# Optimization experiments

Measured on AMD Instinct MI355X. Metric: run time of the kernel, lower is better.

Reference implementation:

```python
import jax, jax.numpy as jnp
import numpy as np
from jax import lax

J = 2  # number of decomposition levels (init arg)


def afb1d(x, h0, h1, axis):
    """1D analysis filter bank along `axis` (2=D, 3=H, 4=W) of NCDHW x.
    h0/h1 are length-L time-reversed filters (cross-correlation weights),
    matching the reversed buffers stored by prep_filt_afb3d.
    Returns (N, 2C, ...) with channel layout (C, [lo, hi]).
    """
    C = x.shape[1]
    L = h0.shape[0]
    n = x.shape[axis]
    # pywt.dwt_coeff_len(n, L, mode='zero') == floor((n + L - 1) / 2)
    outsize = (n + L - 1) // 2
    p = 2 * (outsize - 1) - n + L
    pads = [(0, 0)] * 3
    # torch code: if p odd, pad 1 extra at the END of the axis, then p//2 both sides
    pads[axis - 2] = (p // 2, p // 2 + (p % 2))
    # depthwise weight: interleaved [lo_c, hi_c] per channel group -> (2C, 1, kD, kH, kW)
    w = jnp.tile(jnp.stack([h0, h1]), (C, 1))  # (2C, L)
    kshape = [1, 1, 1]
    kshape[axis - 2] = L
    w = w.reshape(2 * C, 1, *kshape)
    strides = [1, 1, 1]
    strides[axis - 2] = 2
    return lax.conv_general_dilated(
        x, w,
        window_strides=tuple(strides),
        padding=pads,
        feature_group_count=C,
        dimension_numbers=('NCDHW', 'OIDHW', 'NCDHW'),
    )


def dwt3d_level(x, h0, h1):
    """Single-level 3D DWT: row (W), then col (H), then depth (D) filtering."""
    y = afb1d(x, h0, h1, 4)   # along W -> channels (C, 2w)
    y = afb1d(y, h0, h1, 3)   # along H -> channels (C, 2w, 2h)
    y = afb1d(y, h0, h1, 2)   # along D -> channels (C, 2w, 2h, 2d)
    s = y.shape
    y = y.reshape(s[0], -1, 8, s[2], s[3], s[4])  # (N, C, 8, D', H', W')
    low = y[:, :, 0]        # LLL
    highs = y[:, :, 1:]     # 7 high subbands
    return low, highs


def setup_inputs() -> dict:
    key = jax.random.key(0)
    x = jax.random.normal(key, (2, 4, 128, 128, 128), dtype=jnp.float32)
    s = np.float32(1.0 / np.sqrt(2.0))
    # db1 analysis filters, time-reversed (as stored by prep_filt_afb3d):
    # pywt dec_lo=[s,s] -> reversed [s,s]; dec_hi=[-s,s] -> reversed [s,-s]
    h0 = jnp.asarray(np.array([s, s], dtype=np.float32))
    h1 = jnp.asarray(np.array([s, -s], dtype=np.float32))
    return {"x": x, "h0": h0, "h1": h1}


def reference(x, h0, h1):
    ll = x
    yh = []
    for _ in range(J):
        ll, high = dwt3d_level(ll, h0, h1)
        yh.append(high)
    # (lowpass, highs_level0, highs_level1)
    return (ll, *yh)
```

## Files before the change

kernel.cpp:

```cpp
#include <hip/hip_runtime.h>

#define DIM 128
#define NCV 8

__global__ __launch_bounds__(256)
void haar3d_fused(const float* __restrict__ x,
                  const float* __restrict__ h0,
                  const float* __restrict__ h1,
                  float* __restrict__ ll2,
                  float* __restrict__ hi1,
                  float* __restrict__ hi2)
{
    __shared__ float2 lds[4 * 4 * 16];

    const int tw = blockIdx.x;
    const int th = blockIdx.y;
    const int td = blockIdx.z & 15;
    const int nc = blockIdx.z >> 4;

    const int tid = threadIdx.x;
    const int sw2 = tid & 15;
    const int sh  = (tid >> 4) & 3;
    const int sd  = tid >> 6;

    const float g00 = h0[0], g01 = h0[1];
    const float g10 = h1[0], g11 = h1[1];

    const int gd = td * 8 + 2 * sd;
    const int gh = th * 8 + 2 * sh;
    const int gw = tw * 64 + 4 * sw2;

    const float* base = x + ((((long)nc * DIM + gd) * DIM + gh) * DIM + gw);

    float4 q[2][2];
    q[0][0] = *reinterpret_cast<const float4*>(base);
    q[0][1] = *reinterpret_cast<const float4*>(base + DIM);
    q[1][0] = *reinterpret_cast<const float4*>(base + DIM * DIM);
    q[1][1] = *reinterpret_cast<const float4*>(base + DIM * DIM + DIM);

    float Lw[2][2][2], Hw[2][2][2];
#pragma unroll
    for (int i = 0; i < 2; ++i)
#pragma unroll
        for (int j = 0; j < 2; ++j) {
            const float4 v = q[i][j];
            Lw[i][j][0] = g00 * v.x + g01 * v.y;
            Hw[i][j][0] = g10 * v.x + g11 * v.y;
            Lw[i][j][1] = g00 * v.z + g01 * v.w;
            Hw[i][j][1] = g10 * v.z + g11 * v.w;
        }

    float LL[2][2], LH[2][2], HL[2][2], HH[2][2];
#pragma unroll
    for (int i = 0; i < 2; ++i)
#pragma unroll
        for (int s = 0; s < 2; ++s) {
            LL[i][s] = g00 * Lw[i][0][s] + g01 * Lw[i][1][s];
            LH[i][s] = g10 * Lw[i][0][s] + g11 * Lw[i][1][s];
            HL[i][s] = g00 * Hw[i][0][s] + g01 * Hw[i][1][s];
            HH[i][s] = g10 * Hw[i][0][s] + g11 * Hw[i][1][s];
        }

    float LLL[2], LLH[2], LHL[2], LHH[2], HLL[2], HLH[2], HHL[2], HHH[2];
#pragma unroll
    for (int s = 0; s < 2; ++s) {
        LLL[s] = g00 * LL[0][s] + g01 * LL[1][s];
        LLH[s] = g10 * LL[0][s] + g11 * LL[1][s];
        LHL[s] = g00 * LH[0][s] + g01 * LH[1][s];
        LHH[s] = g10 * LH[0][s] + g11 * LH[1][s];
        HLL[s] = g00 * HL[0][s] + g01 * HL[1][s];
        HLH[s] = g10 * HL[0][s] + g11 * HL[1][s];
        HHL[s] = g00 * HH[0][s] + g01 * HH[1][s];
        HHH[s] = g10 * HH[0][s] + g11 * HH[1][s];
    }

    const int d1  = td * 4 + sd;
    const int h1c = th * 4 + sh;
    const int w1  = tw * 32 + 2 * sw2;

    {
        const long S1 = 64L * 64 * 64;
        const long sp = ((long)d1 * 64 + h1c) * 64 + w1;
        float* hb = hi1 + (long)nc * 7 * S1 + sp;
        *reinterpret_cast<float2*>(hb + 0 * S1) = make_float2(LLH[0], LLH[1]);
        *reinterpret_cast<float2*>(hb + 1 * S1) = make_float2(LHL[0], LHL[1]);
        *reinterpret_cast<float2*>(hb + 2 * S1) = make_float2(LHH[0], LHH[1]);
        *reinterpret_cast<float2*>(hb + 3 * S1) = make_float2(HLL[0], HLL[1]);
        *reinterpret_cast<float2*>(hb + 4 * S1) = make_float2(HLH[0], HLH[1]);
        *reinterpret_cast<float2*>(hb + 5 * S1) = make_float2(HHL[0], HHL[1]);
        *reinterpret_cast<float2*>(hb + 6 * S1) = make_float2(HHH[0], HHH[1]);
    }

    lds[(sd * 4 + sh) * 16 + sw2] = make_float2(LLL[0], LLL[1]);

    __syncthreads();

    if (tid < 64) {
        const int zw = tid & 15;
        const int zh = (tid >> 4) & 1;
        const int zd = tid >> 5;

        float Lw2[2][2], Hw2[2][2];
#pragma unroll
        for (int i = 0; i < 2; ++i)
#pragma unroll
            for (int j = 0; j < 2; ++j) {
                const float2 p = lds[((2 * zd + i) * 4 + (2 * zh + j)) * 16 + zw];
                Lw2[i][j] = g00 * p.x + g01 * p.y;
                Hw2[i][j] = g10 * p.x + g11 * p.y;
            }

        float LL2v[2], LH2[2], HL2[2], HH2[2];
#pragma unroll
        for (int i = 0; i < 2; ++i) {
            LL2v[i] = g00 * Lw2[i][0] + g01 * Lw2[i][1];
            LH2[i]  = g10 * Lw2[i][0] + g11 * Lw2[i][1];
            HL2[i]  = g00 * Hw2[i][0] + g01 * Hw2[i][1];
            HH2[i]  = g10 * Hw2[i][0] + g11 * Hw2[i][1];
        }

        const float vLLL = g00 * LL2v[0] + g01 * LL2v[1];
        const float vLLH = g10 * LL2v[0] + g11 * LL2v[1];
        const float vLHL = g00 * LH2[0]  + g01 * LH2[1];
        const float vLHH = g10 * LH2[0]  + g11 * LH2[1];
        const float vHLL = g00 * HL2[0]  + g01 * HL2[1];
        const float vHLH = g10 * HL2[0]  + g11 * HL2[1];
        const float vHHL = g00 * HH2[0]  + g01 * HH2[1];
        const float vHHH = g10 * HH2[0]  + g11 * HH2[1];

        const int d2 = td * 2 + zd;
        const int h2 = th * 2 + zh;
        const int w2 = tw * 16 + zw;

        ll2[(((long)nc * 32 + d2) * 32 + h2) * 32 + w2] = vLLL;

        const long S2 = 32L * 32 * 32;
        const long sp2 = ((long)d2 * 32 + h2) * 32 + w2;
        float* hb2 = hi2 + (long)nc * 7 * S2 + sp2;
        hb2[0 * S2] = vLLH;
        hb2[1 * S2] = vLHL;
        hb2[2 * S2] = vLHH;
        hb2[3 * S2] = vHLL;
        hb2[4 * S2] = vHLH;
        hb2[5 * S2] = vHHL;
        hb2[6 * S2] = vHHH;
    }
}

extern "C" void kernel_launch(void* const* d_in, const int* in_sizes, int n_in,
                              void* d_out, int out_size, void* d_ws, size_t ws_size,
                              hipStream_t stream) {
    const float* x  = (const float*)d_in[0];
    const float* h0 = (const float*)d_in[1];
    const float* h1 = (const float*)d_in[2];
    float* out = (float*)d_out;

    const long LL2_SZ = (long)NCV * 32 * 32 * 32;
    const long H1_SZ  = (long)NCV * 7 * 64 * 64 * 64;
    float* ll2 = out;
    float* hi1 = out + LL2_SZ;
    float* hi2 = out + LL2_SZ + H1_SZ;

    dim3 grid(2, 16, 16 * NCV);
    haar3d_fused<<<grid, 256, 0, stream>>>(x, h0, h1, ll2, hi1, hi2);
}
```

Measured before the change: 114.1 us.

## Cover full W rows per block with 16B stores and nontemporal memory ops

```diff
diff --git a/kernel.cpp b/kernel.cpp
--- a/kernel.cpp
+++ b/kernel.cpp
@@ -2,6 +2,9 @@
 
 #define DIM 128
 #define NCV 8
+
+using f32x4 = __attribute__((ext_vector_type(4))) float;
+using f32x2 = __attribute__((ext_vector_type(2))) float;
 
 __global__ __launch_bounds__(256)
 void haar3d_fused(const float* __restrict__ x,
@@ -11,15 +14,14 @@
                   float* __restrict__ hi1,
                   float* __restrict__ hi2)
 {
-    __shared__ float2 lds[4 * 4 * 16];
+    __shared__ f32x2 lds[4 * 4 * 32];
 
-    const int tw = blockIdx.x;
-    const int th = blockIdx.y;
-    const int td = blockIdx.z & 15;
-    const int nc = blockIdx.z >> 4;
+    const int th = blockIdx.x;
+    const int td = blockIdx.y;
+    const int nc = blockIdx.z;
 
     const int tid = threadIdx.x;
-    const int sw2 = tid & 15;
+    const int swq = tid & 15;
     const int sh  = (tid >> 4) & 3;
     const int sd  = tid >> 6;
 
@@ -28,86 +30,96 @@
 
     const int gd = td * 8 + 2 * sd;
     const int gh = th * 8 + 2 * sh;
-    const int gw = tw * 64 + 4 * sw2;
+    const int gw = 8 * swq;
 
     const float* base = x + ((((long)nc * DIM + gd) * DIM + gh) * DIM + gw);
 
-    float4 q[2][2];
-    q[0][0] = *reinterpret_cast<const float4*>(base);
-    q[0][1] = *reinterpret_cast<const float4*>(base + DIM);
-    q[1][0] = *reinterpret_cast<const float4*>(base + DIM * DIM);
-    q[1][1] = *reinterpret_cast<const float4*>(base + DIM * DIM + DIM);
-
-    float Lw[2][2][2], Hw[2][2][2];
+    f32x4 q[2][2][2];
 #pragma unroll
     for (int i = 0; i < 2; ++i)
 #pragma unroll
         for (int j = 0; j < 2; ++j) {
-            const float4 v = q[i][j];
-            Lw[i][j][0] = g00 * v.x + g01 * v.y;
-            Hw[i][j][0] = g10 * v.x + g11 * v.y;
-            Lw[i][j][1] = g00 * v.z + g01 * v.w;
-            Hw[i][j][1] = g10 * v.z + g11 * v.w;
+            const f32x4* r = reinterpret_cast<const f32x4*>(base + i * DIM * DIM + j * DIM);
+            q[i][j][0] = __builtin_nontemporal_load(r);
+            q[i][j][1] = __builtin_nontemporal_load(r + 1);
         }
 
-    float LL[2][2], LH[2][2], HL[2][2], HH[2][2];
+    float Lw[2][2][4], Hw[2][2][4];
 #pragma unroll
     for (int i = 0; i < 2; ++i)
 #pragma unroll
-        for (int s = 0; s < 2; ++s) {
+        for (int j = 0; j < 2; ++j) {
+            const f32x4 A = q[i][j][0];
+            const f32x4 B = q[i][j][1];
+            Lw[i][j][0] = g00 * A[0] + g01 * A[1];  Hw[i][j][0] = g10 * A[0] + g11 * A[1];
+            Lw[i][j][1] = g00 * A[2] + g01 * A[3];  Hw[i][j][1] = g10 * A[2] + g11 * A[3];
+            Lw[i][j][2] = g00 * B[0] + g01 * B[1];  Hw[i][j][2] = g10 * B[0] + g11 * B[1];
+            Lw[i][j][3] = g00 * B[2] + g01 * B[3];  Hw[i][j][3] = g10 * B[2] + g11 * B[3];
+        }
+
+    float LL[2][4], LH[2][4], HL[2][4], HH[2][4];
+#pragma unroll
+    for (int i = 0; i < 2; ++i)
+#pragma unroll
+        for (int s = 0; s < 4; ++s) {
             LL[i][s] = g00 * Lw[i][0][s] + g01 * Lw[i][1][s];
             LH[i][s] = g10 * Lw[i][0][s] + g11 * Lw[i][1][s];
             HL[i][s] = g00 * Hw[i][0][s] + g01 * Hw[i][1][s];
             HH[i][s] = g10 * Hw[i][0][s] + g11 * Hw[i][1][s];
         }
 
-    float LLL[2], LLH[2], LHL[2], LHH[2], HLL[2], HLH[2], HHL[2], HHH[2];
+    f32x4 vLLL, vLLH, vLHL, vLHH, vHLL, vHLH, vHHL, vHHH;
 #pragma unroll
-    for (int s = 0; s < 2; ++s) {
-        LLL[s] = g00 * LL[0][s] + g01 * LL[1][s];
-        LLH[s] = g10 * LL[0][s] + g11 * LL[1][s];
-        LHL[s] = g00 * LH[0][s] + g01 * LH[1][s];
-        LHH[s] = g10 * LH[0][s] + g11 * LH[1][s];
-        HLL[s] = g00 * HL[0][s] + g01 * HL[1][s];
-        HLH[s] = g10 * HL[0][s] + g11 * HL[1][s];
-        HHL[s] = g00 * HH[0][s] + g01 * HH[1][s];
-        HHH[s] = g10 * HH[0][s] + g11 * HH[1][s];
+    for (int s = 0; s < 4; ++s) {
+        vLLL[s] = g00 * LL[0][s] + g01 * LL[1][s];
+        vLLH[s] = g10 * LL[0][s] + g11 * LL[1][s];
+        vLHL[s] = g00 * LH[0][s] + g01 * LH[1][s];
+        vLHH[s] = g10 * LH[0][s] + g11 * LH[1][s];
+        vHLL[s] = g00 * HL[0][s] + g01 * HL[1][s];
+        vHLH[s] = g10 * HL[0][s] + g11 * HL[1][s];
+        vHHL[s] = g00 * HH[0][s] + g01 * HH[1][s];
+        vHHH[s] = g10 * HH[0][s] + g11 * HH[1][s];
     }
 
     const int d1  = td * 4 + sd;
     const int h1c = th * 4 + sh;
-    const int w1  = tw * 32 + 2 * sw2;
+    const int w1  = 4 * swq;
 
     {
         const long S1 = 64L * 64 * 64;
-        const long sp = ((long)d1 * 64 + h1c) * 64 + w1;
-        float* hb = hi1 + (long)nc * 7 * S1 + sp;
-        *reinterpret_cast<float2*>(hb + 0 * S1) = make_float2(LLH[0], LLH[1]);
-        *reinterpret_cast<float2*>(hb + 1 * S1) = make_float2(LHL[0], LHL[1]);
-        *reinterpret_cast<float2*>(hb + 2 * S1) = make_float2(LHH[0], LHH[1]);
-        *reinterpret_cast<float2*>(hb + 3 * S1) = make_float2(HLL[0], HLL[1]);
-        *reinterpret_cast<float2*>(hb + 4 * S1) = make_float2(HLH[0], HLH[1]);
-        *reinterpret_cast<float2*>(hb + 5 * S1) = make_float2(HHL[0], HHL[1]);
-        *reinterpret_cast<float2*>(hb + 6 * S1) = make_float2(HHH[0], HHH[1]);
+        float* hb = hi1 + (long)nc * 7 * S1 + (((long)d1 * 64 + h1c) * 64 + w1);
+        __builtin_nontemporal_store(vLLH, reinterpret_cast<f32x4*>(hb + 0 * S1));
+        __builtin_nontemporal_store(vLHL, reinterpret_cast<f32x4*>(hb + 1 * S1));
+        __builtin_nontemporal_store(vLHH, reinterpret_cast<f32x4*>(hb + 2 * S1));
+        __builtin_nontemporal_store(vHLL, reinterpret_cast<f32x4*>(hb + 3 * S1));
+        __builtin_nontemporal_store(vHLH, reinterpret_cast<f32x4*>(hb + 4 * S1));
+        __builtin_nontemporal_store(vHHL, reinterpret_cast<f32x4*>(hb + 5 * S1));
+        __builtin_nontemporal_store(vHHH, reinterpret_cast<f32x4*>(hb + 6 * S1));
     }
 
-    lds[(sd * 4 + sh) * 16 + sw2] = make_float2(LLL[0], LLL[1]);
+    {
+        f32x2* dst = &lds[((sd * 4 + sh) * 32) + 2 * swq];
+        f32x2 lo01; lo01[0] = vLLL[0]; lo01[1] = vLLL[1];
+        f32x2 lo23; lo23[0] = vLLL[2]; lo23[1] = vLLL[3];
+        dst[0] = lo01;
+        dst[1] = lo23;
+    }
 
     __syncthreads();
 
-    if (tid < 64) {
-        const int zw = tid & 15;
-        const int zh = (tid >> 4) & 1;
-        const int zd = tid >> 5;
+    if (tid < 128) {
+        const int zw = tid & 31;
+        const int zh = (tid >> 5) & 1;
+        const int zd = tid >> 6;
 
         float Lw2[2][2], Hw2[2][2];
 #pragma unroll
         for (int i = 0; i < 2; ++i)
 #pragma unroll
             for (int j = 0; j < 2; ++j) {
-                const float2 p = lds[((2 * zd + i) * 4 + (2 * zh + j)) * 16 + zw];
-                Lw2[i][j] = g00 * p.x + g01 * p.y;
-                Hw2[i][j] = g10 * p.x + g11 * p.y;
+                const f32x2 p = lds[((2 * zd + i) * 4 + (2 * zh + j)) * 32 + zw];
+                Lw2[i][j] = g00 * p[0] + g01 * p[1];
+                Hw2[i][j] = g10 * p[0] + g11 * p[1];
             }
 
         float LL2v[2], LH2[2], HL2[2], HH2[2];
@@ -119,31 +131,31 @@
             HH2[i]  = g10 * Hw2[i][0] + g11 * Hw2[i][1];
         }
 
-        const float vLLL = g00 * LL2v[0] + g01 * LL2v[1];
-        const float vLLH = g10 * LL2v[0] + g11 * LL2v[1];
-        const float vLHL = g00 * LH2[0]  + g01 * LH2[1];
-        const float vLHH = g10 * LH2[0]  + g11 * LH2[1];
-        const float vHLL = g00 * HL2[0]  + g01 * HL2[1];
-        const float vHLH = g10 * HL2[0]  + g11 * HL2[1];
-        const float vHHL = g00 * HH2[0]  + g01 * HH2[1];
-        const float vHHH = g10 * HH2[0]  + g11 * HH2[1];
+        const float oLLL = g00 * LL2v[0] + g01 * LL2v[1];
+        const float oLLH = g10 * LL2v[0] + g11 * LL2v[1];
+        const float oLHL = g00 * LH2[0]  + g01 * LH2[1];
+        const float oLHH = g10 * LH2[0]  + g11 * LH2[1];
+        const float oHLL = g00 * HL2[0]  + g01 * HL2[1];
+        const float oHLH = g10 * HL2[0]  + g11 * HL2[1];
+        const float oHHL = g00 * HH2[0]  + g01 * HH2[1];
+        const float oHHH = g10 * HH2[0]  + g11 * HH2[1];
 
         const int d2 = td * 2 + zd;
         const int h2 = th * 2 + zh;
-        const int w2 = tw * 16 + zw;
+        const int w2 = zw;
 
-        ll2[(((long)nc * 32 + d2) * 32 + h2) * 32 + w2] = vLLL;
+        __builtin_nontemporal_store(
+            oLLL, &ll2[(((long)nc * 32 + d2) * 32 + h2) * 32 + w2]);
 
         const long S2 = 32L * 32 * 32;
-        const long sp2 = ((long)d2 * 32 + h2) * 32 + w2;
-        float* hb2 = hi2 + (long)nc * 7 * S2 + sp2;
-        hb2[0 * S2] = vLLH;
-        hb2[1 * S2] = vLHL;
-        hb2[2 * S2] = vLHH;
-        hb2[3 * S2] = vHLL;
-        hb2[4 * S2] = vHLH;
-        hb2[5 * S2] = vHHL;
-        hb2[6 * S2] = vHHH;
+        float* hb2 = hi2 + (long)nc * 7 * S2 + (((long)d2 * 32 + h2) * 32 + w2);
+        __builtin_nontemporal_store(oLLH, hb2 + 0 * S2);
+        __builtin_nontemporal_store(oLHL, hb2 + 1 * S2);
+        __builtin_nontemporal_store(oLHH, hb2 + 2 * S2);
+        __builtin_nontemporal_store(oHLL, hb2 + 3 * S2);
+        __builtin_nontemporal_store(oHLH, hb2 + 4 * S2);
+        __builtin_nontemporal_store(oHHL, hb2 + 5 * S2);
+        __builtin_nontemporal_store(oHHH, hb2 + 6 * S2);
     }
 }
 
@@ -161,6 +173,6 @@
     float* hi1 = out + LL2_SZ;
     float* hi2 = out + LL2_SZ + H1_SZ;
 
-    dim3 grid(2, 16, 16 * NCV);
+    dim3 grid(16, 16, NCV);
     haar3d_fused<<<grid, 256, 0, stream>>>(x, h0, h1, ll2, hi1, hi2);
 }
```

Result: slower. 122.4 us (+7.3%).
